# Kernel tuning notes

Hardware: AMD Instinct MI355X
Metric: run time of the kernel (lower is better)

The kernel has to match this reference:

```python
import math
import jax, jax.numpy as jnp
import numpy as np

N, D, E, H = 4096, 512, 64, 8
LN_EPS = 1e-5


def setup_inputs() -> dict:
    key = jax.random.key(0)
    ks = jax.random.split(key, 6)
    return {
        "x": jax.random.normal(ks[0], (N, D), jnp.float32),
        "wq": jax.random.normal(ks[1], (H, D, E), jnp.float32) * 0.05,
        "wk": jax.random.normal(ks[2], (H, D, E), jnp.float32) * 0.05,
        "wv": jax.random.normal(ks[3], (H, D, E), jnp.float32) * 0.05,
        "w_mh": jax.random.normal(ks[4], (H * E, D), jnp.float32) * 0.05,
        "ln1_g": jnp.ones((D,), jnp.float32),
        "ln1_b": jnp.zeros((D,), jnp.float32),
        "ffn_w": jax.random.normal(ks[5], (D, D), jnp.float32) * 0.05,  # torch Linear weight [out,in]
        "ffn_b": jnp.zeros((D,), jnp.float32),
        "ln2_g": jnp.ones((D,), jnp.float32),
        "ln2_b": jnp.zeros((D,), jnp.float32),
    }


def _layernorm(y, g, b):
    m = y.mean(-1, keepdims=True)
    v = ((y - m) ** 2).mean(-1, keepdims=True)
    return (y - m) * jax.lax.rsqrt(v + LN_EPS) * g + b


def reference(x, wq, wk, wv, w_mh, ln1_g, ln1_b, ffn_w, ffn_b, ln2_g, ln2_b):
    dk = math.sqrt(wk.shape[-1])  # sqrt(embedding_size), as in the torch code
    q = jnp.einsum('nd,hde->hne', x, wq)  # [H,N,E]
    k = jnp.einsum('nd,hde->hne', x, wk)
    v = jnp.einsum('nd,hde->hne', x, wv)
    scores = jax.nn.softmax(jnp.einsum('hne,hme->hnm', q, k) / dk, axis=-1)  # [H,N,N]
    z = jnp.einsum('hnm,hme->hne', scores, v)  # [H,N,E]
    concat_z = jnp.transpose(z, (1, 0, 2)).reshape(x.shape[0], -1)  # [N, H*E]
    transformed_z = concat_z @ w_mh  # [N, D]
    normed_z = _layernorm(transformed_z + x, ln1_g, ln1_b)
    out = normed_z @ ffn_w.T + ffn_b  # nn.Linear
    return _layernorm(out + normed_z, ln2_g, ln2_b)
```

## Files before the change

### kernel.cpp

```cpp
#include <hip/hip_runtime.h>

#define NN 4096
#define DD 512
#define EE 64
#define HH 8

typedef _Float16 f16;
typedef f16 f16x4 __attribute__((ext_vector_type(4)));
typedef f16 f16x8 __attribute__((ext_vector_type(8)));
typedef float f32x4 __attribute__((ext_vector_type(4)));

__device__ __forceinline__ float hexp2(float x) { return __builtin_amdgcn_exp2f(x); }

__device__ void tile_transpose_cvt(const float* __restrict__ src, f16* __restrict__ dst,
                                   int R, int C, int bx, int by, int tid)
{
    __shared__ float t[32][33];
    const int tx = tid & 31, ty = tid >> 5;
    #pragma unroll
    for (int i = 0; i < 4; ++i) {
        int r = ty + i * 8;
        t[r][tx] = src[(size_t)(by + r) * C + bx + tx];
    }
    __syncthreads();
    #pragma unroll
    for (int i = 0; i < 4; ++i) {
        int c = ty + i * 8;
        dst[(size_t)(bx + c) * R + by + tx] = (f16)t[tx][c];
    }
}

__global__ __launch_bounds__(256) void prep_kernel(
    const float* __restrict__ x, const float* __restrict__ ffn_w,
    const float* __restrict__ wq, const float* __restrict__ wk, const float* __restrict__ wv,
    const float* __restrict__ w_mh,
    f16* __restrict__ xh, f16* __restrict__ ffnT, f16* __restrict__ wqkvT, f16* __restrict__ wmhT)
{
    const int job = blockIdx.y;
    const int tid = threadIdx.x;
    if (job == 0) {
        size_t i = ((size_t)blockIdx.x * 256 + tid) * 4;
        const size_t step = (size_t)256 * 256 * 4;
        for (; i < (size_t)NN * DD; i += step) {
            float4 t = *(const float4*)(x + i);
            f16x4 h = { (f16)t.x, (f16)t.y, (f16)t.z, (f16)t.w };
            *(f16x4*)(xh + i) = h;
        }
    } else if (job == 1) {
        size_t i = ((size_t)blockIdx.x * 256 + tid) * 4;
        float4 t = *(const float4*)(ffn_w + i);
        f16x4 h = { (f16)t.x, (f16)t.y, (f16)t.z, (f16)t.w };
        *(f16x4*)(ffnT + i) = h;
    } else if (job <= 4) {
        const float* src = (job == 2) ? wq : (job == 3) ? wk : wv;
        f16* dst = wqkvT + (size_t)(job - 2) * HH * EE * DD;
        const int z = blockIdx.x >> 5;
        const int tile = blockIdx.x & 31;
        tile_transpose_cvt(src + (size_t)z * DD * EE, dst + (size_t)z * DD * EE,
                           DD, EE, (tile & 1) * 32, (tile >> 1) * 32, tid);
    } else {
        const int tile = blockIdx.x;
        tile_transpose_cvt(w_mh, wmhT, DD, DD, (tile & 15) * 32, (tile >> 4) * 32, tid);
    }
}

__global__ __launch_bounds__(256) void qkv_mfma_kernel(
    const f16* __restrict__ A, const f16* __restrict__ BT,
    f16* __restrict__ qh, f16* __restrict__ kh, f16* __restrict__ vTh)
{
    __shared__ f16 As[2][64][72];
    __shared__ f16 Bs[2][64][72];
    const int tid = threadIdx.x;
    const int n0 = blockIdx.x * 64;
    const int cb = blockIdx.y;
    const int sel = cb >> 3, h = cb & 7;
    const f16* Arow = A + (size_t)n0 * DD;
    const f16* Brow = BT + (size_t)cb * 64 * DD;

    const int lane = tid & 63, wave = tid >> 6;
    const int l16 = lane & 15, quad = lane >> 4;
    const int m0 = wave * 16;

    const int r1 = tid >> 3, c1 = (tid & 7) * 8;
    const int r2 = (tid + 256) >> 3, c2 = ((tid + 256) & 7) * 8;

    f32x4 acc[4];
    #pragma unroll
    for (int t = 0; t < 4; ++t) acc[t] = (f32x4){0.f, 0.f, 0.f, 0.f};

    f16x8 a1 = *(const f16x8*)(Arow + (size_t)r1 * DD + c1);
    f16x8 a2 = *(const f16x8*)(Arow + (size_t)r2 * DD + c2);
    f16x8 b1 = *(const f16x8*)(Brow + (size_t)r1 * DD + c1);
    f16x8 b2 = *(const f16x8*)(Brow + (size_t)r2 * DD + c2);

    int buf = 0;
    for (int kt = 0; kt < DD; kt += 64) {
        *(f16x8*)(&As[buf][r1][c1]) = a1;
        *(f16x8*)(&As[buf][r2][c2]) = a2;
        *(f16x8*)(&Bs[buf][r1][c1]) = b1;
        *(f16x8*)(&Bs[buf][r2][c2]) = b2;
        __syncthreads();
        if (kt + 64 < DD) {
            a1 = *(const f16x8*)(Arow + (size_t)r1 * DD + kt + 64 + c1);
            a2 = *(const f16x8*)(Arow + (size_t)r2 * DD + kt + 64 + c2);
            b1 = *(const f16x8*)(Brow + (size_t)r1 * DD + kt + 64 + c1);
            b2 = *(const f16x8*)(Brow + (size_t)r2 * DD + kt + 64 + c2);
        }
        #pragma unroll
        for (int kk = 0; kk < 64; kk += 32) {
            f16x8 a = *(const f16x8*)(&As[buf][m0 + l16][kk + quad * 8]);
            #pragma unroll
            for (int t = 0; t < 4; ++t) {
                f16x8 b = *(const f16x8*)(&Bs[buf][t * 16 + l16][kk + quad * 8]);
                acc[t] = __builtin_amdgcn_mfma_f32_16x16x32_f16(a, b, acc[t], 0, 0, 0);
            }
        }
        buf ^= 1;
    }

    if (sel == 2) {
        #pragma unroll
        for (int t = 0; t < 4; ++t) {
            int e = t * 16 + l16;
            f16x4 v = { (f16)acc[t][0], (f16)acc[t][1], (f16)acc[t][2], (f16)acc[t][3] };
            *(f16x4*)(vTh + ((size_t)h * EE + e) * NN + n0 + m0 + quad * 4) = v;
        }
    } else {
        f16* o = (sel == 0) ? qh : kh;
        const float s = (sel == 0) ? 0.125f * 1.44269504088896f : 1.0f;
        #pragma unroll
        for (int r = 0; r < 4; ++r) {
            int row = n0 + m0 + quad * 4 + r;
            #pragma unroll
            for (int t = 0; t < 4; ++t)
                o[(size_t)h * NN * EE + (size_t)row * EE + t * 16 + l16] = (f16)(acc[t][r] * s);
        }
    }
}

#define BQ 128
#define BK 64
#define LK (BK + 12)

__global__ __launch_bounds__(256) void attn_mfma_kernel(
    const f16* __restrict__ q, const f16* __restrict__ k,
    const f16* __restrict__ vT, f16* __restrict__ Opart, float* __restrict__ lpart)
{
    __shared__ f16 Ks[2][BK][LK];
    __shared__ f16 VsT[2][EE][LK];

    const int tid = threadIdx.x;
    const int h = blockIdx.y;
    const int n0 = blockIdx.x * BQ;
    const int sp = blockIdx.z;
    const int nsp = gridDim.z;
    const int wave = tid >> 6;
    const int lane = tid & 63;
    const int l16 = lane & 15;
    const int quad = lane >> 4;
    const int m0 = wave * 16;

    const f16* qh = q + (size_t)h * NN * EE;
    const f16* kh = k + (size_t)h * NN * EE;
    const f16* vh = vT + (size_t)h * NN * EE;

    f16x8 qf[2][2];
    #pragma unroll
    for (int s = 0; s < 2; ++s) {
        const f16* qb = qh + (size_t)(n0 + s * 64 + m0 + l16) * EE;
        qf[s][0] = *(const f16x8*)(qb + quad * 8);
        qf[s][1] = *(const f16x8*)(qb + 32 + quad * 8);
    }

    float lp[2] = {0.f, 0.f};
    f32x4 O[2][4];
    #pragma unroll
    for (int s = 0; s < 2; ++s)
        #pragma unroll
        for (int t = 0; t < 4; ++t) O[s][t] = (f32x4){0.f, 0.f, 0.f, 0.f};

    const int span = NN / nsp;
    const int k_begin = sp * span;
    const int k_end = k_begin + span;

    const int srow = tid >> 3, sc8 = (tid & 7) * 8;
    const int srow2 = (tid + 256) >> 3, sc82 = ((tid + 256) & 7) * 8;
    #define KPERM(kk_) (((kk_) & 0x23) | (((kk_) & 0x04) << 2) | (((kk_) & 0x18) >> 1))
    const int prow1 = KPERM(srow), prow2 = KPERM(srow2);

    f16x8 kr0 = *(const f16x8*)(kh + (size_t)(k_begin + srow) * EE + sc8);
    f16x8 kr1 = *(const f16x8*)(kh + (size_t)(k_begin + srow2) * EE + sc82);
    f16x8 vr0 = *(const f16x8*)(vh + (size_t)srow * NN + k_begin + sc8);
    f16x8 vr1 = *(const f16x8*)(vh + (size_t)srow2 * NN + k_begin + sc82);

    int buf = 0;
    for (int kt = k_begin; kt < k_end; kt += BK) {
        *(f16x8*)(&Ks[buf][prow1][sc8]) = kr0;
        *(f16x8*)(&Ks[buf][prow2][sc82]) = kr1;
        *(f16x8*)(&VsT[buf][srow][sc8]) = vr0;
        *(f16x8*)(&VsT[buf][srow2][sc82]) = vr1;
        __syncthreads();

        if (kt + BK < k_end) {
            kr0 = *(const f16x8*)(kh + (size_t)(kt + BK + srow) * EE + sc8);
            kr1 = *(const f16x8*)(kh + (size_t)(kt + BK + srow2) * EE + sc82);
            vr0 = *(const f16x8*)(vh + (size_t)srow * NN + kt + BK + sc8);
            vr1 = *(const f16x8*)(vh + (size_t)srow2 * NN + kt + BK + sc82);
        }

        f16x8 bf[2][2];
        #pragma unroll
        for (int t = 0; t < 4; ++t) {
            f16x8 a0 = *(const f16x8*)(&Ks[buf][t * 16 + l16][quad * 8]);
            f16x8 a1 = *(const f16x8*)(&Ks[buf][t * 16 + l16][32 + quad * 8]);
            #pragma unroll
            for (int s = 0; s < 2; ++s) {
                f32x4 st = {0.f, 0.f, 0.f, 0.f};
                st = __builtin_amdgcn_mfma_f32_16x16x32_f16(a0, qf[s][0], st, 0, 0, 0);
                st = __builtin_amdgcn_mfma_f32_16x16x32_f16(a1, qf[s][1], st, 0, 0, 0);
                float p0 = hexp2(st[0]);
                float p1 = hexp2(st[1]);
                float p2 = hexp2(st[2]);
                float p3 = hexp2(st[3]);
                lp[s] += (p0 + p1) + (p2 + p3);
                f16x8& b = bf[s][t >> 1];
                const int o = (t & 1) * 4;
                b[o + 0] = (f16)p0; b[o + 1] = (f16)p1;
                b[o + 2] = (f16)p2; b[o + 3] = (f16)p3;
            }
        }

        #pragma unroll
        for (int te = 0; te < 4; ++te) {
            f16x8 v0 = *(const f16x8*)(&VsT[buf][te * 16 + l16][quad * 8]);
            f16x8 v1 = *(const f16x8*)(&VsT[buf][te * 16 + l16][32 + quad * 8]);
            #pragma unroll
            for (int s = 0; s < 2; ++s) {
                O[s][te] = __builtin_amdgcn_mfma_f32_16x16x32_f16(v0, bf[s][0], O[s][te], 0, 0, 0);
                O[s][te] = __builtin_amdgcn_mfma_f32_16x16x32_f16(v1, bf[s][1], O[s][te], 0, 0, 0);
            }
        }
        buf ^= 1;
    }

    #pragma unroll
    for (int s = 0; s < 2; ++s) {
        float l = lp[s];
        l += __shfl_xor(l, 16);
        l += __shfl_xor(l, 32);
        const int row = n0 + s * 64 + m0 + l16;
        if (quad == 0)
            lpart[(size_t)sp * HH * NN + (size_t)h * NN + row] = l;
        const float inv = 1.f / l;
        f16* obase = Opart + ((size_t)sp * NN + row) * DD + h * EE;
        #pragma unroll
        for (int te = 0; te < 4; ++te) {
            f16x4 v = { (f16)(O[s][te][0] * inv), (f16)(O[s][te][1] * inv),
                        (f16)(O[s][te][2] * inv), (f16)(O[s][te][3] * inv) };
            *(f16x4*)(obase + te * 16 + quad * 4) = v;
        }
    }
}

__global__ __launch_bounds__(256) void attn_combine_kernel(
    const f16* __restrict__ Opart, const float* __restrict__ lpart, f16* __restrict__ zh, int nsp)
{
    const size_t idx = ((size_t)blockIdx.x * 256 + threadIdx.x) * 8;
    const int n = (int)(idx >> 9);
    const int h = (int)((idx & 511) >> 6);
    float lw[8];
    float lsum = 0.f;
    for (int s = 0; s < nsp; ++s) {
        lw[s] = lpart[(size_t)s * HH * NN + (size_t)h * NN + n];
        lsum += lw[s];
    }
    const float inv = 1.f / lsum;
    float acc[8];
    #pragma unroll
    for (int i = 0; i < 8; ++i) acc[i] = 0.f;
    for (int s = 0; s < nsp; ++s) {
        f16x8 o = *(const f16x8*)(Opart + (size_t)s * NN * DD + idx);
        const float w = lw[s] * inv;
        #pragma unroll
        for (int i = 0; i < 8; ++i) acc[i] += w * (float)o[i];
    }
    f16x8 z;
    #pragma unroll
    for (int i = 0; i < 8; ++i) z[i] = (f16)acc[i];
    *(f16x8*)(zh + idx) = z;
}

__global__ __launch_bounds__(256) void gemm_mfma_kernel(
    const f16* __restrict__ A, const f16* __restrict__ BT,
    const float* __restrict__ bias, const f16* __restrict__ resid16,
    f16* __restrict__ out)
{
    __shared__ f16 As[2][64][72];
    __shared__ f16 Bs[2][64][72];
    const int tid = threadIdx.x;
    const int n0 = blockIdx.x * 64;
    const int j0 = blockIdx.y * 64;
    const f16* Arow = A + (size_t)n0 * DD;
    const f16* Brow = BT + (size_t)j0 * DD;

    const int lane = tid & 63, wave = tid >> 6;
    const int l16 = lane & 15, quad = lane >> 4;
    const int m0 = wave * 16;

    const int r1 = tid >> 3, c1 = (tid & 7) * 8;
    const int r2 = (tid + 256) >> 3, c2 = ((tid + 256) & 7) * 8;

    f32x4 acc[4];
    #pragma unroll
    for (int t = 0; t < 4; ++t) acc[t] = (f32x4){0.f, 0.f, 0.f, 0.f};

    f16x8 a1 = *(const f16x8*)(Arow + (size_t)r1 * DD + c1);
    f16x8 a2 = *(const f16x8*)(Arow + (size_t)r2 * DD + c2);
    f16x8 b1 = *(const f16x8*)(Brow + (size_t)r1 * DD + c1);
    f16x8 b2 = *(const f16x8*)(Brow + (size_t)r2 * DD + c2);

    int buf = 0;
    for (int kt = 0; kt < DD; kt += 64) {
        *(f16x8*)(&As[buf][r1][c1]) = a1;
        *(f16x8*)(&As[buf][r2][c2]) = a2;
        *(f16x8*)(&Bs[buf][r1][c1]) = b1;
        *(f16x8*)(&Bs[buf][r2][c2]) = b2;
        __syncthreads();
        if (kt + 64 < DD) {
            a1 = *(const f16x8*)(Arow + (size_t)r1 * DD + kt + 64 + c1);
            a2 = *(const f16x8*)(Arow + (size_t)r2 * DD + kt + 64 + c2);
            b1 = *(const f16x8*)(Brow + (size_t)r1 * DD + kt + 64 + c1);
            b2 = *(const f16x8*)(Brow + (size_t)r2 * DD + kt + 64 + c2);
        }
        #pragma unroll
        for (int kk = 0; kk < 64; kk += 32) {
            f16x8 a = *(const f16x8*)(&As[buf][m0 + l16][kk + quad * 8]);
            #pragma unroll
            for (int t = 0; t < 4; ++t) {
                f16x8 b = *(const f16x8*)(&Bs[buf][t * 16 + l16][kk + quad * 8]);
                acc[t] = __builtin_amdgcn_mfma_f32_16x16x32_f16(a, b, acc[t], 0, 0, 0);
            }
        }
        buf ^= 1;
    }

    #pragma unroll
    for (int r = 0; r < 4; ++r) {
        int row = n0 + m0 + quad * 4 + r;
        #pragma unroll
        for (int t = 0; t < 4; ++t) {
            int col = j0 + t * 16 + l16;
            float v = acc[t][r];
            if (bias)    v += bias[col];
            if (resid16) v += (float)resid16[(size_t)row * DD + col];
            out[(size_t)row * DD + col] = (f16)v;
        }
    }
}

__global__ __launch_bounds__(256) void ln_kernel(
    const f16* __restrict__ y, const float* __restrict__ g, const float* __restrict__ b,
    f16* __restrict__ oh, float* __restrict__ of)
{
    const int lane = threadIdx.x & 63, wave = threadIdx.x >> 6;
    const int row = blockIdx.x * 4 + wave;
    f16x8 v = *(const f16x8*)(y + (size_t)row * DD + lane * 8);
    float vf[8];
    float s = 0.f, q = 0.f;
    #pragma unroll
    for (int i = 0; i < 8; ++i) {
        vf[i] = (float)v[i];
        s += vf[i];
        q += vf[i] * vf[i];
    }
    #pragma unroll
    for (int o = 1; o < 64; o <<= 1) { s += __shfl_xor(s, o); q += __shfl_xor(q, o); }
    float mean = s * (1.f / DD);
    float var = q * (1.f / DD) - mean * mean;
    float inv = rsqrtf(var + 1e-5f);

    f32x4 g0 = *(const f32x4*)(g + lane * 8);
    f32x4 g1 = *(const f32x4*)(g + lane * 8 + 4);
    f32x4 b0 = *(const f32x4*)(b + lane * 8);
    f32x4 b1 = *(const f32x4*)(b + lane * 8 + 4);
    float o8[8];
    #pragma unroll
    for (int i = 0; i < 4; ++i) {
        o8[i]     = (vf[i] - mean) * inv * g0[i] + b0[i];
        o8[i + 4] = (vf[i + 4] - mean) * inv * g1[i] + b1[i];
    }
    if (oh) {
        f16x8 hv;
        #pragma unroll
        for (int i = 0; i < 8; ++i) hv[i] = (f16)o8[i];
        *(f16x8*)(oh + (size_t)row * DD + lane * 8) = hv;
    }
    if (of) {
        f32x4 f0 = { o8[0], o8[1], o8[2], o8[3] };
        f32x4 f1 = { o8[4], o8[5], o8[6], o8[7] };
        *(f32x4*)(of + (size_t)row * DD + lane * 8) = f0;
        *(f32x4*)(of + (size_t)row * DD + lane * 8 + 4) = f1;
    }
}

extern "C" void kernel_launch(void* const* d_in, const int* in_sizes, int n_in,
                              void* d_out, int out_size, void* d_ws, size_t ws_size,
                              hipStream_t stream) {
    const float* x     = (const float*)d_in[0];
    const float* wq    = (const float*)d_in[1];
    const float* wk    = (const float*)d_in[2];
    const float* wv    = (const float*)d_in[3];
    const float* w_mh  = (const float*)d_in[4];
    const float* ln1_g = (const float*)d_in[5];
    const float* ln1_b = (const float*)d_in[6];
    const float* ffn_w = (const float*)d_in[7];
    const float* ffn_b = (const float*)d_in[8];
    const float* ln2_g = (const float*)d_in[9];
    const float* ln2_b = (const float*)d_in[10];
    float* out = (float*)d_out;

    const size_t poolBytes = ((size_t)3 * HH * EE * DD + 2 * (size_t)DD * DD
                            + 3 * (size_t)HH * NN * EE + 3 * (size_t)NN * DD) * 2;
    int SP = 2;
    {
        size_t need4 = (size_t)4 * NN * DD * 2 + (size_t)4 * HH * NN * 4 + poolBytes + 4096;
        if (ws_size >= need4) SP = 4;
    }

    char* base = (char*)d_ws;
    f16* Opart = (f16*)base;
    float* lpart = (float*)(base + (size_t)SP * NN * DD * 2);
    f16* y16  = (f16*)base;
    size_t regionA = (size_t)SP * NN * DD * 2 + (size_t)SP * HH * NN * 4;
    regionA = (regionA + 255) & ~(size_t)255;
    f16* p = (f16*)(base + regionA);
    f16* wqkvT  = p; p += (size_t)3 * HH * EE * DD;
    f16* wmhT   = p; p += (size_t)DD * DD;
    f16* ffnT   = p; p += (size_t)DD * DD;
    f16* qh     = p; p += (size_t)HH * NN * EE;
    f16* kh     = p; p += (size_t)HH * NN * EE;
    f16* vTh    = p; p += (size_t)HH * NN * EE;
    f16* zh     = p; p += (size_t)NN * DD;
    f16* nzh    = p; p += (size_t)NN * DD;
    f16* xh     = p; p += (size_t)NN * DD;

    prep_kernel<<<dim3(256, 6), 256, 0, stream>>>(x, ffn_w, wq, wk, wv, w_mh,
                                                  xh, ffnT, wqkvT, wmhT);

    qkv_mfma_kernel<<<dim3(NN / 64, 24), 256, 0, stream>>>(xh, wqkvT, qh, kh, vTh);
    attn_mfma_kernel<<<dim3(NN / BQ, HH, SP), 256, 0, stream>>>(qh, kh, vTh, Opart, lpart);
    attn_combine_kernel<<<dim3(NN * DD / 2048), 256, 0, stream>>>(Opart, lpart, zh, SP);
    gemm_mfma_kernel<<<dim3(NN / 64, DD / 64), 256, 0, stream>>>(zh, wmhT, nullptr, xh, y16);
    ln_kernel<<<dim3(NN / 4), 256, 0, stream>>>(y16, ln1_g, ln1_b, nzh, nullptr);
    gemm_mfma_kernel<<<dim3(NN / 64, DD / 64), 256, 0, stream>>>(nzh, ffnT, ffn_b, nzh, y16);
    ln_kernel<<<dim3(NN / 4), 256, 0, stream>>>(y16, ln2_g, ln2_b, nullptr, out);
}
```

Measured before the change: 179.6 us.

## Fuse split-K attention combine into output projection GEMM and single-buffer attention LDS

Removes the separate attn_combine kernel. The output-projection GEMM now reads the per-split partial outputs and row sums directly and combines them while staging its A tile into LDS. The attention kernel drops its double-buffered K/V shared tiles for a single buffer plus an extra barrier, and uses packed round-toward-zero f16 conversions. This saves one launch and one write and read of the combined z buffer. In exchange, each output-column block now rereads the partial outputs (8x redundant combine work), the attention loop gains a barrier, and RTZ rounding changes numerics slightly.

```diff
diff --git a/kernel.cpp b/kernel.cpp
--- a/kernel.cpp
+++ b/kernel.cpp
@@ -6,11 +6,18 @@
 #define HH 8
 
 typedef _Float16 f16;
+typedef f16 f16x2 __attribute__((ext_vector_type(2)));
 typedef f16 f16x4 __attribute__((ext_vector_type(4)));
 typedef f16 f16x8 __attribute__((ext_vector_type(8)));
 typedef float f32x4 __attribute__((ext_vector_type(4)));
+typedef __fp16 fp16x2 __attribute__((ext_vector_type(2)));
 
 __device__ __forceinline__ float hexp2(float x) { return __builtin_amdgcn_exp2f(x); }
+__device__ __forceinline__ f16x2 pkrtz(float a, float b) {
+    fp16x2 r = __builtin_amdgcn_cvt_pkrtz(a, b);
+    return __builtin_bit_cast(f16x2, r);
+}
+union f16x4u { f16x4 v4; f16x2 v2[2]; };
 
 __device__ void tile_transpose_cvt(const float* __restrict__ src, f16* __restrict__ dst,
                                    int R, int C, int bx, int by, int tid)
@@ -146,8 +153,8 @@
     const f16* __restrict__ q, const f16* __restrict__ k,
     const f16* __restrict__ vT, f16* __restrict__ Opart, float* __restrict__ lpart)
 {
-    __shared__ f16 Ks[2][BK][LK];
-    __shared__ f16 VsT[2][EE][LK];
+    __shared__ f16 Ks[BK][LK];
+    __shared__ f16 VsT[EE][LK];
 
     const int tid = threadIdx.x;
     const int h = blockIdx.y;
@@ -193,12 +200,12 @@
     f16x8 vr0 = *(const f16x8*)(vh + (size_t)srow * NN + k_begin + sc8);
     f16x8 vr1 = *(const f16x8*)(vh + (size_t)srow2 * NN + k_begin + sc82);
 
-    int buf = 0;
     for (int kt = k_begin; kt < k_end; kt += BK) {
-        *(f16x8*)(&Ks[buf][prow1][sc8]) = kr0;
-        *(f16x8*)(&Ks[buf][prow2][sc82]) = kr1;
-        *(f16x8*)(&VsT[buf][srow][sc8]) = vr0;
-        *(f16x8*)(&VsT[buf][srow2][sc82]) = vr1;
+        __syncthreads();
+        *(f16x8*)(&Ks[prow1][sc8]) = kr0;
+        *(f16x8*)(&Ks[prow2][sc82]) = kr1;
+        *(f16x8*)(&VsT[srow][sc8]) = vr0;
+        *(f16x8*)(&VsT[srow2][sc82]) = vr1;
         __syncthreads();
 
         if (kt + BK < k_end) {
@@ -211,8 +218,8 @@
         f16x8 bf[2][2];
         #pragma unroll
         for (int t = 0; t < 4; ++t) {
-            f16x8 a0 = *(const f16x8*)(&Ks[buf][t * 16 + l16][quad * 8]);
-            f16x8 a1 = *(const f16x8*)(&Ks[buf][t * 16 + l16][32 + quad * 8]);
+            f16x8 a0 = *(const f16x8*)(&Ks[t * 16 + l16][quad * 8]);
+            f16x8 a1 = *(const f16x8*)(&Ks[t * 16 + l16][32 + quad * 8]);
             #pragma unroll
             for (int s = 0; s < 2; ++s) {
                 f32x4 st = {0.f, 0.f, 0.f, 0.f};
@@ -223,24 +230,23 @@
                 float p2 = hexp2(st[2]);
                 float p3 = hexp2(st[3]);
                 lp[s] += (p0 + p1) + (p2 + p3);
-                f16x8& b = bf[s][t >> 1];
-                const int o = (t & 1) * 4;
-                b[o + 0] = (f16)p0; b[o + 1] = (f16)p1;
-                b[o + 2] = (f16)p2; b[o + 3] = (f16)p3;
+                f16x2* bp = (f16x2*)&bf[s][t >> 1];
+                const int o2 = (t & 1) * 2;
+                bp[o2 + 0] = pkrtz(p0, p1);
+                bp[o2 + 1] = pkrtz(p2, p3);
             }
         }
 
         #pragma unroll
         for (int te = 0; te < 4; ++te) {
-            f16x8 v0 = *(const f16x8*)(&VsT[buf][te * 16 + l16][quad * 8]);
-            f16x8 v1 = *(const f16x8*)(&VsT[buf][te * 16 + l16][32 + quad * 8]);
+            f16x8 v0 = *(const f16x8*)(&VsT[te * 16 + l16][quad * 8]);
+            f16x8 v1 = *(const f16x8*)(&VsT[te * 16 + l16][32 + quad * 8]);
             #pragma unroll
             for (int s = 0; s < 2; ++s) {
                 O[s][te] = __builtin_amdgcn_mfma_f32_16x16x32_f16(v0, bf[s][0], O[s][te], 0, 0, 0);
                 O[s][te] = __builtin_amdgcn_mfma_f32_16x16x32_f16(v1, bf[s][1], O[s][te], 0, 0, 0);
             }
         }
-        buf ^= 1;
     }
 
     #pragma unroll
@@ -255,39 +261,105 @@
         f16* obase = Opart + ((size_t)sp * NN + row) * DD + h * EE;
         #pragma unroll
         for (int te = 0; te < 4; ++te) {
-            f16x4 v = { (f16)(O[s][te][0] * inv), (f16)(O[s][te][1] * inv),
-                        (f16)(O[s][te][2] * inv), (f16)(O[s][te][3] * inv) };
-            *(f16x4*)(obase + te * 16 + quad * 4) = v;
-        }
-    }
-}
-
-__global__ __launch_bounds__(256) void attn_combine_kernel(
-    const f16* __restrict__ Opart, const float* __restrict__ lpart, f16* __restrict__ zh, int nsp)
-{
-    const size_t idx = ((size_t)blockIdx.x * 256 + threadIdx.x) * 8;
-    const int n = (int)(idx >> 9);
-    const int h = (int)((idx & 511) >> 6);
-    float lw[8];
-    float lsum = 0.f;
+            f16x4u v;
+            v.v2[0] = pkrtz(O[s][te][0] * inv, O[s][te][1] * inv);
+            v.v2[1] = pkrtz(O[s][te][2] * inv, O[s][te][3] * inv);
+            *(f16x4*)(obase + te * 16 + quad * 4) = v.v4;
+        }
+    }
+}
+
+__global__ __launch_bounds__(256) void gemmz_mfma_kernel(
+    const f16* __restrict__ Opart, const float* __restrict__ lpart, int nsp,
+    const f16* __restrict__ BT, const f16* __restrict__ resid16, f16* __restrict__ out)
+{
+    __shared__ f16 As[2][64][72];
+    __shared__ f16 Bs[2][64][72];
+    const int tid = threadIdx.x;
+    const int n0 = blockIdx.x * 64;
+    const int j0 = blockIdx.y * 64;
+    const f16* Brow = BT + (size_t)j0 * DD;
+
+    const int lane = tid & 63, wave = tid >> 6;
+    const int l16 = lane & 15, quad = lane >> 4;
+    const int m0 = wave * 16;
+
+    const int r1 = tid >> 3, c1 = (tid & 7) * 8;
+    const int r2 = (tid + 256) >> 3, c2 = ((tid + 256) & 7) * 8;
+
+    f32x4 acc[4];
+    #pragma unroll
+    for (int t = 0; t < 4; ++t) acc[t] = (f32x4){0.f, 0.f, 0.f, 0.f};
+
+    f16x8 op1[4], op2[4];
     for (int s = 0; s < nsp; ++s) {
-        lw[s] = lpart[(size_t)s * HH * NN + (size_t)h * NN + n];
-        lsum += lw[s];
-    }
-    const float inv = 1.f / lsum;
-    float acc[8];
-    #pragma unroll
-    for (int i = 0; i < 8; ++i) acc[i] = 0.f;
-    for (int s = 0; s < nsp; ++s) {
-        f16x8 o = *(const f16x8*)(Opart + (size_t)s * NN * DD + idx);
-        const float w = lw[s] * inv;
-        #pragma unroll
-        for (int i = 0; i < 8; ++i) acc[i] += w * (float)o[i];
-    }
-    f16x8 z;
-    #pragma unroll
-    for (int i = 0; i < 8; ++i) z[i] = (f16)acc[i];
-    *(f16x8*)(zh + idx) = z;
+        op1[s] = *(const f16x8*)(Opart + ((size_t)s * NN + n0 + r1) * DD + c1);
+        op2[s] = *(const f16x8*)(Opart + ((size_t)s * NN + n0 + r2) * DD + c2);
+    }
+    f16x8 b1 = *(const f16x8*)(Brow + (size_t)r1 * DD + c1);
+    f16x8 b2 = *(const f16x8*)(Brow + (size_t)r2 * DD + c2);
+
+    int buf = 0;
+    for (int kt = 0; kt < DD; kt += 64) {
+        const int h = kt >> 6;
+        float lw1[4], lw2[4], s1 = 0.f, s2 = 0.f;
+        for (int s = 0; s < nsp; ++s) {
+            lw1[s] = lpart[(size_t)s * HH * NN + (size_t)h * NN + n0 + r1];
+            lw2[s] = lpart[(size_t)s * HH * NN + (size_t)h * NN + n0 + r2];
+            s1 += lw1[s]; s2 += lw2[s];
+        }
+        const float i1 = 1.f / s1, i2 = 1.f / s2;
+        float aw1[8], aw2[8];
+        #pragma unroll
+        for (int i = 0; i < 8; ++i) { aw1[i] = 0.f; aw2[i] = 0.f; }
+        for (int s = 0; s < nsp; ++s) {
+            const float w1 = lw1[s] * i1, w2 = lw2[s] * i2;
+            #pragma unroll
+            for (int i = 0; i < 8; ++i) {
+                aw1[i] += w1 * (float)op1[s][i];
+                aw2[i] += w2 * (float)op2[s][i];
+            }
+        }
+        f16x2* a1p = (f16x2*)(&As[buf][r1][c1]);
+        f16x2* a2p = (f16x2*)(&As[buf][r2][c2]);
+        #pragma unroll
+        for (int i = 0; i < 4; ++i) {
+            a1p[i] = pkrtz(aw1[2 * i], aw1[2 * i + 1]);
+            a2p[i] = pkrtz(aw2[2 * i], aw2[2 * i + 1]);
+        }
+        *(f16x8*)(&Bs[buf][r1][c1]) = b1;
+        *(f16x8*)(&Bs[buf][r2][c2]) = b2;
+        __syncthreads();
+        if (kt + 64 < DD) {
+            for (int s = 0; s < nsp; ++s) {
+                op1[s] = *(const f16x8*)(Opart + ((size_t)s * NN + n0 + r1) * DD + kt + 64 + c1);
+                op2[s] = *(const f16x8*)(Opart + ((size_t)s * NN + n0 + r2) * DD + kt + 64 + c2);
+            }
+            b1 = *(const f16x8*)(Brow + (size_t)r1 * DD + kt + 64 + c1);
+            b2 = *(const f16x8*)(Brow + (size_t)r2 * DD + kt + 64 + c2);
+        }
+        #pragma unroll
+        for (int kk = 0; kk < 64; kk += 32) {
+            f16x8 a = *(const f16x8*)(&As[buf][m0 + l16][kk + quad * 8]);
+            #pragma unroll
+            for (int t = 0; t < 4; ++t) {
+                f16x8 b = *(const f16x8*)(&Bs[buf][t * 16 + l16][kk + quad * 8]);
+                acc[t] = __builtin_amdgcn_mfma_f32_16x16x32_f16(a, b, acc[t], 0, 0, 0);
+            }
+        }
+        buf ^= 1;
+    }
+
+    #pragma unroll
+    for (int r = 0; r < 4; ++r) {
+        int row = n0 + m0 + quad * 4 + r;
+        #pragma unroll
+        for (int t = 0; t < 4; ++t) {
+            int col = j0 + t * 16 + l16;
+            float v = acc[t][r] + (float)resid16[(size_t)row * DD + col];
+            out[(size_t)row * DD + col] = (f16)v;
+        }
+    }
 }
 
 __global__ __launch_bounds__(256) void gemm_mfma_kernel(
@@ -430,7 +502,6 @@
     char* base = (char*)d_ws;
     f16* Opart = (f16*)base;
     float* lpart = (float*)(base + (size_t)SP * NN * DD * 2);
-    f16* y16  = (f16*)base;
     size_t regionA = (size_t)SP * NN * DD * 2 + (size_t)SP * HH * NN * 4;
     regionA = (regionA + 255) & ~(size_t)255;
     f16* p = (f16*)(base + regionA);
@@ -440,7 +511,7 @@
     f16* qh     = p; p += (size_t)HH * NN * EE;
     f16* kh     = p; p += (size_t)HH * NN * EE;
     f16* vTh    = p; p += (size_t)HH * NN * EE;
-    f16* zh     = p; p += (size_t)NN * DD;
+    f16* y16    = p; p += (size_t)NN * DD;
     f16* nzh    = p; p += (size_t)NN * DD;
     f16* xh     = p; p += (size_t)NN * DD;
 
@@ -449,8 +520,7 @@
 
     qkv_mfma_kernel<<<dim3(NN / 64, 24), 256, 0, stream>>>(xh, wqkvT, qh, kh, vTh);
     attn_mfma_kernel<<<dim3(NN / BQ, HH, SP), 256, 0, stream>>>(qh, kh, vTh, Opart, lpart);
-    attn_combine_kernel<<<dim3(NN * DD / 2048), 256, 0, stream>>>(Opart, lpart, zh, SP);
-    gemm_mfma_kernel<<<dim3(NN / 64, DD / 64), 256, 0, stream>>>(zh, wmhT, nullptr, xh, y16);
+    gemmz_mfma_kernel<<<dim3(NN / 64, DD / 64), 256, 0, stream>>>(Opart, lpart, SP, wmhT, xh, y16);
     ln_kernel<<<dim3(NN / 4), 256, 0, stream>>>(y16, ln1_g, ln1_b, nzh, nullptr);
     gemm_mfma_kernel<<<dim3(NN / 64, DD / 64), 256, 0, stream>>>(nzh, ffnT, ffn_b, nzh, y16);
     ln_kernel<<<dim3(NN / 4), 256, 0, stream>>>(y16, ln2_g, ln2_b, nullptr, out);
```

Result: slower. 319.5 us (+77.9%).
